# Optimization experiments

Hardware: AMD Instinct MI355X
Metric: run time of the kernel (lower is better)

The kernel has to match this reference:

```python
import jax, jax.numpy as jnp
import numpy as np

EPS = 1e-5
K = 20

def lrelu(x):
    return jnp.where(x >= 0, x, 0.2 * x)

def in2d(x):  # [B,C,N,k] instance norm over (N,k), no affine, biased var
    m = jnp.mean(x, axis=(2, 3), keepdims=True)
    v = jnp.var(x, axis=(2, 3), keepdims=True)
    return (x - m) * jax.lax.rsqrt(v + EPS)

def in1d(x):  # [B,C,N] instance norm over N
    m = jnp.mean(x, axis=2, keepdims=True)
    v = jnp.var(x, axis=2, keepdims=True)
    return (x - m) * jax.lax.rsqrt(v + EPS)

def knn_idx(x, k):  # x: [B,C,N]; uses only first 3 channels (as original)
    p = x[:, :3, :]
    inner = -2.0 * jnp.einsum('bcn,bcm->bnm', p, p)
    xx = jnp.sum(p * p, axis=1)  # [B,N]
    pd = -xx[:, :, None] - inner - xx[:, None, :]  # negative squared dist [B,N,N]
    return jax.lax.top_k(pd, k)[1]  # [B,N,k]

def graph_feature(x, k):  # x: [B,C,N] -> [B,2C,N,k]
    idx = knn_idx(x, k)
    xT = jnp.transpose(x, (0, 2, 1))  # [B,N,C]
    feat = jax.vmap(lambda t, i: t[i])(xT, idx)  # [B,N,k,C]
    center = xT[:, :, None, :]
    out = jnp.concatenate([feat - center, jnp.broadcast_to(center, feat.shape)], axis=3)
    return jnp.transpose(out, (0, 3, 1, 2))  # [B,2C,N,k]

def conv2d1(w, x):  # 1x1 conv2d: w [O,C], x [B,C,N,k]
    return jnp.einsum('oc,bcnk->bonk', w, x)

def conv1d1(w, x):  # 1x1 conv1d: w [O,C], x [B,C,N]
    return jnp.einsum('oc,bcn->bon', w, x)

def setup_inputs() -> dict:
    key = jax.random.key(0)
    ks = jax.random.split(key, 10)
    def w(k, o, c):
        return jax.random.normal(k, (o, c), dtype=jnp.float32) * np.float32(1.0 / np.sqrt(c))
    return {
        'x':  jax.random.normal(ks[0], (4, 4096, 4), dtype=jnp.float32),
        'w1': w(ks[1], 64, 8),
        'w2': w(ks[2], 64, 64),
        'w3': w(ks[3], 64, 128),
        'w4': w(ks[4], 64, 64),
        'w5': w(ks[5], 64, 128),
        'w6': w(ks[6], 1024, 192),
        'w7': w(ks[7], 512, 1216),
        'w8': w(ks[8], 256, 512),
        'w9': w(ks[9], 2, 256),
    }

def reference(x, w1, w2, w3, w4, w5, w6, w7, w8, w9):
    xt = jnp.transpose(x, (0, 2, 1))  # [B,4,N]
    num_points = xt.shape[2]
    # EdgeConv block 1
    f = graph_feature(xt, K)                     # [B,8,N,k]
    h = lrelu(in2d(conv2d1(w1, f)))
    h = lrelu(in2d(conv2d1(w2, h)))
    x1 = jnp.max(h, axis=-1)                     # [B,64,N]
    # EdgeConv block 2
    f = graph_feature(x1, K)                     # [B,128,N,k]
    h = lrelu(in2d(conv2d1(w3, f)))
    h = lrelu(in2d(conv2d1(w4, h)))
    x2 = jnp.max(h, axis=-1)
    # EdgeConv block 3
    f = graph_feature(x2, K)
    h = lrelu(in2d(conv2d1(w5, f)))
    x3 = jnp.max(h, axis=-1)
    # global embedding
    cat = jnp.concatenate([x1, x2, x3], axis=1)  # [B,192,N]
    g = lrelu(in1d(conv1d1(w6, cat)))            # [B,1024,N]
    g = jnp.max(g, axis=-1, keepdims=True)       # [B,1024,1]
    g = jnp.broadcast_to(g, (g.shape[0], g.shape[1], num_points))
    h = jnp.concatenate([g, x1, x2, x3], axis=1) # [B,1216,N]
    h = lrelu(in1d(conv1d1(w7, h)))
    h = lrelu(in1d(conv1d1(w8, h)))
    # dropout identity (eval mode)
    out = conv1d1(w9, h)                         # [B,2,N]
    return jnp.transpose(out, (0, 2, 1))         # [B,N,2]
```

## Files before the change

kernel.cpp:

```cpp
#include <hip/hip_runtime.h>
#include <hip/hip_fp16.h>
#include <math.h>

constexpr int BB  = 4;
constexpr int NN  = 4096;
constexpr int KK  = 20;
constexpr int NKK = NN * KK;
constexpr int TPOS = BB * NKK;
constexpr int NMASK = NN - 1;

#define DEVFN __device__ __forceinline__

DEVFN float lrelu_f(float v) { return v >= 0.f ? v : 0.2f * v; }
DEVFN unsigned fenc(float f) { unsigned u = __float_as_uint(f); return (u & 0x80000000u) ? ~u : (u | 0x80000000u); }
DEVFN float fdec(unsigned k) { unsigned u = (k & 0x80000000u) ? (k & 0x7fffffffu) : ~k; return __uint_as_float(u); }

template<int CSTRIDE>
__global__ __launch_bounds__(256) void knn_kernel(const float* __restrict__ xin, int* __restrict__ idxout)
{
    __shared__ float sx[NN], sy[NN], sz[NN];
    __shared__ unsigned sdist[NN];
    __shared__ unsigned shist[256];
    __shared__ unsigned scollv[256];
    __shared__ unsigned long long scoll64[128];
    __shared__ unsigned sres[2];
    __shared__ unsigned scnt[2];
    const int tid = threadIdx.x;
    const int b  = blockIdx.x >> 8;
    const int q0 = (blockIdx.x & 255) * 16;
    for (int i = tid; i < NN; i += 256) {
        const float4 rc = *reinterpret_cast<const float4*>(xin + (size_t)(b*NN + i) * CSTRIDE);
        sx[i] = rc.x; sy[i] = rc.y; sz[i] = rc.z;
    }

    for (int qq = 0; qq < 16; ++qq) {
        __syncthreads();
        shist[tid] = 0;
        if (tid == 0) { scnt[0] = 0; scnt[1] = 0; }
        const int qi = q0 + qq;
        const float qx = sx[qi], qy = sy[qi], qz = sz[qi];
        const float nxx = -__fadd_rn(__fadd_rn(__fmul_rn(qx,qx), __fmul_rn(qy,qy)), __fmul_rn(qz,qz));
        __syncthreads();
#pragma unroll
        for (int i = 0; i < NN/256; ++i) {
            const int m = tid + (i << 8);
            float cx = sx[m], cy = sy[m], cz = sz[m];
            float cw  = __fadd_rn(__fadd_rn(__fmul_rn(cx,cx), __fmul_rn(cy,cy)), __fmul_rn(cz,cz));
            float dot = __fadd_rn(__fadd_rn(__fmul_rn(qx,cx), __fmul_rn(qy,cy)), __fmul_rn(qz,cz));
            float pd  = __fsub_rn(__fsub_rn(nxx, __fmul_rn(-2.f, dot)), cw);
            unsigned u = fenc(pd);
            sdist[m] = u;
            atomicAdd(&shist[u >> 24], 1u);
        }
        __syncthreads();
        if (tid < 64) {
            const int base = 255 - tid*4;
            unsigned h0 = shist[base], h1 = shist[base-1], h2 = shist[base-2], h3 = shist[base-3];
            unsigned s = h0 + h1 + h2 + h3;
            unsigned c = s;
#pragma unroll
            for (int off = 1; off < 64; off <<= 1) { unsigned t = __shfl_up(c, off, 64); if (tid >= off) c += t; }
            unsigned cprev = c - s;
            if (c >= KK && cprev < KK) {
                unsigned cc = cprev; int bb = base;
                if (cc + h0 < KK) { cc += h0; bb = base-1;
                    if (cc + h1 < KK) { cc += h1; bb = base-2;
                        if (cc + h2 < KK) { cc += h2; bb = base-3; } } }
                sres[0] = (unsigned)bb; sres[1] = KK - cc;
            }
        }
        __syncthreads();
        const unsigned b0 = sres[0], K1 = sres[1];
        shist[tid] = 0;
        __syncthreads();
#pragma unroll
        for (int i = 0; i < NN/256; ++i) {
            unsigned u = sdist[tid + (i << 8)];
            if ((u >> 24) == b0) atomicAdd(&shist[(u >> 16) & 255u], 1u);
        }
        __syncthreads();
        if (tid < 64) {
            const int base = 255 - tid*4;
            unsigned h0 = shist[base], h1 = shist[base-1], h2 = shist[base-2], h3 = shist[base-3];
            unsigned s = h0 + h1 + h2 + h3;
            unsigned c = s;
#pragma unroll
            for (int off = 1; off < 64; off <<= 1) { unsigned t = __shfl_up(c, off, 64); if (tid >= off) c += t; }
            unsigned cprev = c - s;
            if (c >= K1 && cprev < K1) {
                unsigned cc = cprev; int bb = base;
                if (cc + h0 < K1) { cc += h0; bb = base-1;
                    if (cc + h1 < K1) { cc += h1; bb = base-2;
                        if (cc + h2 < K1) { cc += h2; bb = base-3; } } }
                sres[0] = (unsigned)bb; sres[1] = K1 - cc;
            }
        }
        __syncthreads();
        const unsigned prefix16 = (b0 << 8) | sres[0];
        const unsigned K2 = sres[1];
#pragma unroll
        for (int i = 0; i < NN/256; ++i) {
            unsigned u = sdist[tid + (i << 8)];
            if ((u >> 16) == prefix16) {
                unsigned pos = atomicAdd(&scnt[0], 1u);
                if (pos < 256u) scollv[pos] = u;
            }
        }
        __syncthreads();
        {
            int cb = (int)scnt[0]; if (cb > 256) cb = 256;
            if (tid < cb) {
                unsigned v = scollv[tid];
                unsigned ng = 0, ne = 0;
                for (int j = 0; j < cb; ++j) {
                    unsigned w = scollv[j];
                    ng += (w > v); ne += (w == v);
                }
                if (ng < K2 && ng + ne >= K2) sres[0] = v;
            }
        }
        __syncthreads();
        const unsigned W = sres[0];
#pragma unroll
        for (int i = 0; i < NN/256; ++i) {
            const int m = tid + (i << 8);
            unsigned u = sdist[m];
            if (u >= W) {
                unsigned pos = atomicAdd(&scnt[1], 1u);
                if (pos < 128u) scoll64[pos] = ((unsigned long long)u << 32) | (unsigned)(NN-1 - m);
            }
        }
        __syncthreads();
        {
            int c2 = (int)scnt[1]; if (c2 > 128) c2 = 128;
            if (tid < c2) {
                unsigned long long kv = scoll64[tid];
                int rank = 0;
                for (int j = 0; j < c2; ++j) rank += (scoll64[j] > kv);
                if (rank < KK) {
                    int* op = idxout + ((size_t)(b*NN + qi)) * KK;
                    op[rank] = (NN-1) - (int)(kv & 0xFFFFFFFFull);
                }
            }
        }
    }
}

template<int CINH, int CSTRIDE>
__global__ __launch_bounds__(64) void uv_kernel(const float* __restrict__ xin, const float* __restrict__ w,
                                                float* __restrict__ ub, float* __restrict__ vb)
{
    __shared__ float sp[32][CINH];
    const int lane = threadIdx.x;
    float wa[CINH], wd[CINH];
#pragma unroll
    for (int c = 0; c < CINH; ++c) {
        float a = w[lane*(2*CINH) + c];
        wa[c] = a;
        wd[c] = w[lane*(2*CINH) + CINH + c] - a;
    }
    const int p0 = blockIdx.x * 32;
    for (int i = lane; i < 32*CINH; i += 64) {
        int pi = i / CINH, c = i % CINH;
        sp[pi][c] = xin[(size_t)(p0 + pi)*CSTRIDE + c];
    }
    __syncthreads();
    for (int pi = 0; pi < 32; ++pi) {
        float au = 0.f, av = 0.f;
#pragma unroll
        for (int c = 0; c < CINH; ++c) {
            float xv = sp[pi][c];
            au = fmaf(wa[c], xv, au);
            av = fmaf(wd[c], xv, av);
        }
        ub[(size_t)(p0 + pi)*64 + lane] = au;
        vb[(size_t)(p0 + pi)*64 + lane] = av;
    }
}

template<bool STOREMAX>
__global__ __launch_bounds__(64) void gstat_kernel(const float* __restrict__ ub, const float* __restrict__ vb,
    const int* __restrict__ idx, float* __restrict__ xraw,
    double* __restrict__ ssum, double* __restrict__ ssq)
{
    const int lane = threadIdx.x;
    const int g0 = blockIdx.x * 8;
    const int b = g0 / NN;
    double lsum = 0.0, lsq = 0.0;
    for (int ni = 0; ni < 8; ++ni) {
        const int g = g0 + ni;
        const float v = vb[(size_t)g*64 + lane];
        float vmax = -INFINITY;
        for (int k = 0; k < KK; ++k) {
            const int j = idx[(size_t)g*KK + k] & NMASK;
            float o = ub[(size_t)(b*NN + j)*64 + lane] + v;
            if constexpr (STOREMAX) vmax = fmaxf(vmax, o);
            lsum += (double)o; lsq += (double)o*(double)o;
        }
        if constexpr (STOREMAX) xraw[(size_t)g*64 + lane] = vmax;
    }
    atomicAdd(&ssum[b*64+lane], lsum);
    atomicAdd(&ssq [b*64+lane], lsq);
}

__global__ __launch_bounds__(64) void s1b_kernel(const float* __restrict__ x, const int* __restrict__ idx,
    const float* __restrict__ w1, const float* __restrict__ w2,
    const float* __restrict__ m1, const float* __restrict__ r1,
    float* __restrict__ xraw, double* __restrict__ ssum, double* __restrict__ ssq)
{
    __shared__ float sh[64];
    const int lane = threadIdx.x;
    float wr1[8];
#pragma unroll
    for (int c = 0; c < 8; ++c) wr1[c] = w1[lane*8 + c];
    float wr2[64];
#pragma unroll
    for (int c = 0; c < 64; ++c) wr2[c] = w2[lane*64 + c];
    const int g0 = blockIdx.x * 8;
    const int b = g0 / NN;
    const float mm = m1[b*64+lane], rr = r1[b*64+lane];
    double lsum = 0.0, lsq = 0.0;
    for (int ni = 0; ni < 8; ++ni) {
        const int g = g0 + ni;
        const float4 ct = *reinterpret_cast<const float4*>(x + (size_t)g*4);
        float vmax = -INFINITY;
        for (int k = 0; k < KK; ++k) {
            const int j = idx[(size_t)g*KK + k] & NMASK;
            const float4 nb = *reinterpret_cast<const float4*>(x + (size_t)(b*NN + j)*4);
            float o1 = wr1[0]*(nb.x-ct.x) + wr1[1]*(nb.y-ct.y) + wr1[2]*(nb.z-ct.z) + wr1[3]*(nb.w-ct.w)
                     + wr1[4]*ct.x + wr1[5]*ct.y + wr1[6]*ct.z + wr1[7]*ct.w;
            float h = lrelu_f((o1 - mm) * rr);
            __syncthreads();
            sh[lane] = h;
            __syncthreads();
            float acc = 0.f;
#pragma unroll
            for (int c = 0; c < 64; c += 4) {
                const float4 hv = *reinterpret_cast<const float4*>(&sh[c]);
                acc += wr2[c]*hv.x + wr2[c+1]*hv.y + wr2[c+2]*hv.z + wr2[c+3]*hv.w;
            }
            vmax = fmaxf(vmax, acc);
            lsum += (double)acc; lsq += (double)acc*(double)acc;
        }
        xraw[(size_t)g*64 + lane] = vmax;
    }
    atomicAdd(&ssum[b*64+lane], lsum);
    atomicAdd(&ssq [b*64+lane], lsq);
}

__global__ __launch_bounds__(64) void s2b_kernel(const float* __restrict__ xin, const int* __restrict__ idx,
    const float* __restrict__ w3, const float* __restrict__ w4,
    const float* __restrict__ m3, const float* __restrict__ r3,
    float* __restrict__ xraw, double* __restrict__ ssum, double* __restrict__ ssq)
{
    __shared__ float sf[128];
    __shared__ float sh[64];
    const int lane = threadIdx.x;
    float wr3[128];
#pragma unroll
    for (int c = 0; c < 128; ++c) wr3[c] = w3[lane*128 + c];
    float wr4[64];
#pragma unroll
    for (int c = 0; c < 64; ++c) wr4[c] = w4[lane*64 + c];
    const int g0 = blockIdx.x * 8;
    const int b = g0 / NN;
    const float mm = m3[b*64+lane], rr = r3[b*64+lane];
    double lsum = 0.0, lsq = 0.0;
    for (int ni = 0; ni < 8; ++ni) {
        const int g = g0 + ni;
        const float ctl = xin[(size_t)g*64 + lane];
        float vmax = -INFINITY;
        for (int k = 0; k < KK; ++k) {
            const int j = idx[(size_t)g*KK + k] & NMASK;
            const float nbl = xin[(size_t)(b*NN + j)*64 + lane];
            __syncthreads();
            sf[lane] = nbl - ctl;
            sf[64+lane] = ctl;
            __syncthreads();
            float o3 = 0.f;
#pragma unroll
            for (int c = 0; c < 128; c += 4) {
                const float4 fv = *reinterpret_cast<const float4*>(&sf[c]);
                o3 += wr3[c]*fv.x + wr3[c+1]*fv.y + wr3[c+2]*fv.z + wr3[c+3]*fv.w;
            }
            float h = lrelu_f((o3 - mm) * rr);
            __syncthreads();
            sh[lane] = h;
            __syncthreads();
            float acc = 0.f;
#pragma unroll
            for (int c = 0; c < 64; c += 4) {
                const float4 hv = *reinterpret_cast<const float4*>(&sh[c]);
                acc += wr4[c]*hv.x + wr4[c+1]*hv.y + wr4[c+2]*hv.z + wr4[c+3]*hv.w;
            }
            vmax = fmaxf(vmax, acc);
            lsum += (double)acc; lsq += (double)acc*(double)acc;
        }
        xraw[(size_t)g*64 + lane] = vmax;
    }
    atomicAdd(&ssum[b*64+lane], lsum);
    atomicAdd(&ssq [b*64+lane], lsq);
}

__global__ void fin_kernel(const double* __restrict__ ssum, const double* __restrict__ ssq,
                           float* __restrict__ meanp, float* __restrict__ rstdp, int total, double invn)
{
    int t = blockIdx.x*256 + threadIdx.x;
    if (t >= total) return;
    double m = ssum[t]*invn;
    double v = ssq[t]*invn - m*m;
    meanp[t] = (float)m;
    rstdp[t] = (float)(1.0 / sqrt(v + 1e-5));
}

__global__ void finx_kernel(float* __restrict__ xv, const float* __restrict__ m, const float* __restrict__ r)
{
    int t = blockIdx.x*256 + threadIdx.x;
    int c0 = (t & 15) * 4;
    int b = t >> 16;
    float4 v = *reinterpret_cast<float4*>(xv + (size_t)t*4);
    v.x = lrelu_f((v.x - m[b*64+c0+0]) * r[b*64+c0+0]);
    v.y = lrelu_f((v.y - m[b*64+c0+1]) * r[b*64+c0+1]);
    v.z = lrelu_f((v.z - m[b*64+c0+2]) * r[b*64+c0+2]);
    v.w = lrelu_f((v.w - m[b*64+c0+3]) * r[b*64+c0+3]);
    *reinterpret_cast<float4*>(xv + (size_t)t*4) = v;
}

__global__ void transw_kernel(const float* __restrict__ w, float* __restrict__ wT, int O, int C, int rs, int off)
{
    int t = blockIdx.x*256 + threadIdx.x;
    if (t >= O*C) return;
    int o = t % O, c = t / O;
    wT[t] = w[(size_t)o*rs + off + c];
}

__global__ __launch_bounds__(256) void conv6_kernel(
    const float* __restrict__ x1, const float* __restrict__ x2, const float* __restrict__ x3,
    const float* __restrict__ wT, double* __restrict__ s6sum, double* __restrict__ s6sq, unsigned* __restrict__ s6max)
{
    __shared__ float si[32][192];
    const int b = blockIdx.z, nbase = blockIdx.x*32;
    const int o = blockIdx.y*256 + threadIdx.x;
    for (int i = threadIdx.x; i < 32*192; i += 256) {
        int nl = i/192, c = i%192;
        size_t base = (size_t)(b*NN + nbase + nl)*64;
        si[nl][c] = (c < 64) ? x1[base + c] : (c < 128) ? x2[base + c - 64] : x3[base + c - 128];
    }
    __syncthreads();
    float acc[32];
#pragma unroll
    for (int n = 0; n < 32; ++n) acc[n] = 0.f;
    for (int c = 0; c < 192; ++c) {
        float wv = wT[(size_t)c*1024 + o];
#pragma unroll
        for (int n = 0; n < 32; ++n) acc[n] = fmaf(wv, si[n][c], acc[n]);
    }
    double ps = 0.0, pq = 0.0; float pm = -INFINITY;
#pragma unroll
    for (int n = 0; n < 32; ++n) { ps += (double)acc[n]; pq += (double)acc[n]*(double)acc[n]; pm = fmaxf(pm, acc[n]); }
    atomicAdd(&s6sum[b*1024+o], ps);
    atomicAdd(&s6sq [b*1024+o], pq);
    atomicMax(&s6max[b*1024+o], fenc(pm));
}

__global__ void gfin_kernel(const double* __restrict__ s6sum, const double* __restrict__ s6sq,
                            const unsigned* __restrict__ s6max, float* __restrict__ g)
{
    int t = blockIdx.x*256 + threadIdx.x;
    double m = s6sum[t] * (1.0/4096.0);
    double v = s6sq[t] * (1.0/4096.0) - m*m;
    float rs = (float)(1.0 / sqrt(v + 1e-5));
    g[t] = lrelu_f((fdec(s6max[t]) - (float)m) * rs);
}

__global__ __launch_bounds__(256) void gbias_kernel(const float* __restrict__ w7, const float* __restrict__ g,
                                                    float* __restrict__ gbias)
{
    const int b = blockIdx.y;
    const int o = blockIdx.x*256 + threadIdx.x;
    const float* wr = w7 + (size_t)o*1216;
    const float* gv = g + b*1024;
    float acc = 0.f;
    for (int c = 0; c < 1024; c += 4) {
        float4 wv = *reinterpret_cast<const float4*>(&wr[c]);
        float4 gg = *reinterpret_cast<const float4*>(&gv[c]);
        acc = fmaf(wv.x, gg.x, fmaf(wv.y, gg.y, fmaf(wv.z, gg.z, fmaf(wv.w, gg.w, acc))));
    }
    gbias[b*512+o] = acc;
}

__global__ __launch_bounds__(256) void conv7a_kernel(
    const float* __restrict__ x1, const float* __restrict__ x2, const float* __restrict__ x3,
    const float* __restrict__ wT, const float* __restrict__ gbias,
    __half* __restrict__ out7h, double* __restrict__ ssum, double* __restrict__ ssq)
{
    __shared__ float si[32][192];
    const int b = blockIdx.z, nbase = blockIdx.x*32;
    const int o = blockIdx.y*256 + threadIdx.x;
    for (int i = threadIdx.x; i < 32*192; i += 256) {
        int nl = i/192, c = i%192;
        size_t base = (size_t)(b*NN + nbase + nl)*64;
        si[nl][c] = (c < 64) ? x1[base + c] : (c < 128) ? x2[base + c - 64] : x3[base + c - 128];
    }
    __syncthreads();
    float acc[32];
    const float gb = gbias[b*512 + o];
#pragma unroll
    for (int n = 0; n < 32; ++n) acc[n] = gb;
    for (int c = 0; c < 192; ++c) {
        float wv = wT[(size_t)c*512 + o];
#pragma unroll
        for (int n = 0; n < 32; ++n) acc[n] = fmaf(wv, si[n][c], acc[n]);
    }
    double ps = 0.0, pq = 0.0;
#pragma unroll
    for (int n = 0; n < 32; ++n) {
        out7h[(size_t)(b*NN + nbase + n)*512 + o] = __float2half(acc[n]);
        ps += (double)acc[n]; pq += (double)acc[n]*(double)acc[n];
    }
    atomicAdd(&ssum[b*512+o], ps);
    atomicAdd(&ssq [b*512+o], pq);
}

__global__ __launch_bounds__(256) void conv8k_kernel(
    const __half* __restrict__ out7h, const float* __restrict__ m7, const float* __restrict__ r7,
    const float* __restrict__ wT8,
    float* __restrict__ out8, double* __restrict__ ssum, double* __restrict__ ssq)
{
    __shared__ float h7[16][512];
    const int b = blockIdx.y, nbase = blockIdx.x*16;
    const int tid = threadIdx.x;
    for (int i = tid; i < 16*512; i += 256) {
        int nl = i >> 9, c = i & 511;
        float v = __half2float(out7h[(size_t)(b*NN + nbase + nl)*512 + c]);
        h7[nl][c] = lrelu_f((v - m7[b*512+c]) * r7[b*512+c]);
    }
    __syncthreads();
    const int o = tid;
    float acc8[16];
#pragma unroll
    for (int n = 0; n < 16; ++n) acc8[n] = 0.f;
    for (int c = 0; c < 512; ++c) {
        float wv = wT8[(size_t)c*256 + o];
#pragma unroll
        for (int n = 0; n < 16; ++n) acc8[n] = fmaf(wv, h7[n][c], acc8[n]);
    }
    double ps = 0.0, pq = 0.0;
#pragma unroll
    for (int n = 0; n < 16; ++n) {
        out8[(size_t)(b*NN + nbase + n)*256 + o] = acc8[n];
        ps += (double)acc8[n]; pq += (double)acc8[n]*(double)acc8[n];
    }
    atomicAdd(&ssum[b*256+o], ps);
    atomicAdd(&ssq [b*256+o], pq);
}

__global__ __launch_bounds__(256) void conv9_kernel(const float* __restrict__ in8,
    const float* __restrict__ meanp, const float* __restrict__ rstdp,
    const float* __restrict__ w9, float* __restrict__ outp)
{
    const int lane = threadIdx.x & 63, wv = threadIdx.x >> 6;
    const int ng = blockIdx.x*4 + wv;
    const int b = ng / NN;
    const int c0 = lane*4;
    const float4 v4 = *reinterpret_cast<const float4*>(&in8[(size_t)ng*256 + c0]);
    float vv[4] = {v4.x, v4.y, v4.z, v4.w};
    float a0 = 0.f, a1 = 0.f;
#pragma unroll
    for (int i = 0; i < 4; ++i) {
        int c = c0 + i;
        float a = lrelu_f((vv[i] - meanp[b*256+c]) * rstdp[b*256+c]);
        a0 = fmaf(w9[c],     a, a0);
        a1 = fmaf(w9[256+c], a, a1);
    }
#pragma unroll
    for (int off = 32; off > 0; off >>= 1) {
        a0 += __shfl_down(a0, off, 64);
        a1 += __shfl_down(a1, off, 64);
    }
    if (lane == 0) { outp[(size_t)ng*2 + 0] = a0; outp[(size_t)ng*2 + 1] = a1; }
}

extern "C" void kernel_launch(void* const* d_in, const int* in_sizes, int n_in,
                              void* d_out, int out_size, void* d_ws, size_t ws_size,
                              hipStream_t stream)
{
    const float* x  = (const float*)d_in[0];
    const float* w1 = (const float*)d_in[1];
    const float* w2 = (const float*)d_in[2];
    const float* w3 = (const float*)d_in[3];
    const float* w4 = (const float*)d_in[4];
    const float* w5 = (const float*)d_in[5];
    const float* w6 = (const float*)d_in[6];
    const float* w7 = (const float*)d_in[7];
    const float* w8 = (const float*)d_in[8];
    const float* w9 = (const float*)d_in[9];
    float* outp = (float*)d_out;

    char* ws = (char*)d_ws;
    size_t off = 0;
    auto alloc = [&](size_t bytes) -> void* {
        void* p = ws + off;
        off = (off + bytes + 255) & ~(size_t)255;
        return p;
    };
    double* dstats = (double*)alloc((size_t)16896 * 8);
    unsigned* u6max = (unsigned*)alloc((size_t)4096 * 4);
    float* fstats = (float*)alloc((size_t)14848 * 4);
    int*   idxb  = (int*)  alloc((size_t)TPOS * 4);
    float* wT6   = (float*)alloc((size_t)1024*192*4);
    float* wT7   = (float*)alloc((size_t)512*192*4);
    float* wT8   = (float*)alloc((size_t)256*512*4);
    char*  sc17  = (char*) alloc((size_t)BB*NN*512*2);
    float* ubuf  = (float*)sc17;
    float* vbuf  = (float*)(sc17 + (size_t)BB*NN*64*4);
    __half* out7h = (__half*)sc17;
    float* x1v   = (float*)alloc((size_t)BB*NN*64*4);
    float* x2v   = (float*)alloc((size_t)BB*NN*64*4);
    float* x3v   = (float*)alloc((size_t)BB*NN*64*4);
    float* out8  = (float*)alloc((size_t)BB*NN*256*4);

    double* d1 = dstats;           double* d2 = dstats + 512;
    double* d3 = dstats + 1024;    double* d4 = dstats + 1536;
    double* d5 = dstats + 2048;
    double* d6sum = dstats + 2560; double* d6sq = d6sum + 4096;
    double* d7sum = dstats + 10752; double* d7sq = d7sum + 2048;
    double* d8sum = dstats + 14848; double* d8sq = d8sum + 1024;
    float* m1 = fstats;        float* r1 = fstats + 256;
    float* m2 = fstats + 512;  float* r2 = fstats + 768;
    float* m3 = fstats + 1024; float* r3 = fstats + 1280;
    float* m4 = fstats + 1536; float* r4 = fstats + 1792;
    float* m5 = fstats + 2048; float* r5 = fstats + 2304;
    float* g  = fstats + 2560;
    float* m7 = fstats + 6656; float* r7 = fstats + 8704;
    float* gbias = fstats + 10752;
    float* m8 = fstats + 12800; float* r8 = fstats + 13824;

    hipMemsetAsync(dstats, 0, (size_t)16896*8 + (size_t)4096*4, stream);

    transw_kernel<<<768, 256, 0, stream>>>(w6, wT6, 1024, 192, 192, 0);
    transw_kernel<<<384, 256, 0, stream>>>(w7, wT7, 512, 192, 1216, 1024);
    transw_kernel<<<512, 256, 0, stream>>>(w8, wT8, 256, 512, 512, 0);

    knn_kernel<4><<<1024, 256, 0, stream>>>(x, idxb);
    uv_kernel<4, 4><<<512, 64, 0, stream>>>(x, w1, ubuf, vbuf);
    gstat_kernel<false><<<2048, 64, 0, stream>>>(ubuf, vbuf, idxb, nullptr, d1, d1+256);
    fin_kernel<<<1, 256, 0, stream>>>(d1, d1+256, m1, r1, 256, 1.0/81920.0);
    s1b_kernel<<<2048, 64, 0, stream>>>(x, idxb, w1, w2, m1, r1, x1v, d2, d2+256);
    fin_kernel<<<1, 256, 0, stream>>>(d2, d2+256, m2, r2, 256, 1.0/81920.0);
    finx_kernel<<<1024, 256, 0, stream>>>(x1v, m2, r2);

    knn_kernel<64><<<1024, 256, 0, stream>>>(x1v, idxb);
    uv_kernel<64, 64><<<512, 64, 0, stream>>>(x1v, w3, ubuf, vbuf);
    gstat_kernel<false><<<2048, 64, 0, stream>>>(ubuf, vbuf, idxb, nullptr, d3, d3+256);
    fin_kernel<<<1, 256, 0, stream>>>(d3, d3+256, m3, r3, 256, 1.0/81920.0);
    s2b_kernel<<<2048, 64, 0, stream>>>(x1v, idxb, w3, w4, m3, r3, x2v, d4, d4+256);
    fin_kernel<<<1, 256, 0, stream>>>(d4, d4+256, m4, r4, 256, 1.0/81920.0);
    finx_kernel<<<1024, 256, 0, stream>>>(x2v, m4, r4);

    knn_kernel<64><<<1024, 256, 0, stream>>>(x2v, idxb);
    uv_kernel<64, 64><<<512, 64, 0, stream>>>(x2v, w5, ubuf, vbuf);
    gstat_kernel<true><<<2048, 64, 0, stream>>>(ubuf, vbuf, idxb, x3v, d5, d5+256);
    fin_kernel<<<1, 256, 0, stream>>>(d5, d5+256, m5, r5, 256, 1.0/81920.0);
    finx_kernel<<<1024, 256, 0, stream>>>(x3v, m5, r5);

    conv6_kernel<<<dim3(128, 4, 4), 256, 0, stream>>>(x1v, x2v, x3v, wT6, d6sum, d6sq, u6max);
    gfin_kernel<<<16, 256, 0, stream>>>(d6sum, d6sq, u6max, g);
    gbias_kernel<<<dim3(2, 4), 256, 0, stream>>>(w7, g, gbias);

    conv7a_kernel<<<dim3(128, 2, 4), 256, 0, stream>>>(x1v, x2v, x3v, wT7, gbias, out7h, d7sum, d7sq);
    fin_kernel<<<8, 256, 0, stream>>>(d7sum, d7sq, m7, r7, 2048, 1.0/4096.0);
    conv8k_kernel<<<dim3(256, 4), 256, 0, stream>>>(out7h, m7, r7, wT8, out8, d8sum, d8sq);
    fin_kernel<<<4, 256, 0, stream>>>(d8sum, d8sq, m8, r8, 1024, 1.0/4096.0);
    conv9_kernel<<<4096, 256, 0, stream>>>(out8, m8, r8, w9, outp);
}
```

Measured before the change: 1.855 ms.

## Drop global embedding branch cancelled by instance norm; keep kNN keys in registers

```diff
diff --git a/kernel.cpp b/kernel.cpp
--- a/kernel.cpp
+++ b/kernel.cpp
@@ -13,13 +13,11 @@
 
 DEVFN float lrelu_f(float v) { return v >= 0.f ? v : 0.2f * v; }
 DEVFN unsigned fenc(float f) { unsigned u = __float_as_uint(f); return (u & 0x80000000u) ? ~u : (u | 0x80000000u); }
-DEVFN float fdec(unsigned k) { unsigned u = (k & 0x80000000u) ? (k & 0x7fffffffu) : ~k; return __uint_as_float(u); }
 
 template<int CSTRIDE>
 __global__ __launch_bounds__(256) void knn_kernel(const float* __restrict__ xin, int* __restrict__ idxout)
 {
     __shared__ float sx[NN], sy[NN], sz[NN];
-    __shared__ unsigned sdist[NN];
     __shared__ unsigned shist[256];
     __shared__ unsigned scollv[256];
     __shared__ unsigned long long scoll64[128];
@@ -41,6 +39,7 @@
         const float qx = sx[qi], qy = sy[qi], qz = sz[qi];
         const float nxx = -__fadd_rn(__fadd_rn(__fmul_rn(qx,qx), __fmul_rn(qy,qy)), __fmul_rn(qz,qz));
         __syncthreads();
+        unsigned ukey[NN/256];
 #pragma unroll
         for (int i = 0; i < NN/256; ++i) {
             const int m = tid + (i << 8);
@@ -49,7 +48,7 @@
             float dot = __fadd_rn(__fadd_rn(__fmul_rn(qx,cx), __fmul_rn(qy,cy)), __fmul_rn(qz,cz));
             float pd  = __fsub_rn(__fsub_rn(nxx, __fmul_rn(-2.f, dot)), cw);
             unsigned u = fenc(pd);
-            sdist[m] = u;
+            ukey[i] = u;
             atomicAdd(&shist[u >> 24], 1u);
         }
         __syncthreads();
@@ -75,7 +74,7 @@
         __syncthreads();
 #pragma unroll
         for (int i = 0; i < NN/256; ++i) {
-            unsigned u = sdist[tid + (i << 8)];
+            unsigned u = ukey[i];
             if ((u >> 24) == b0) atomicAdd(&shist[(u >> 16) & 255u], 1u);
         }
         __syncthreads();
@@ -100,7 +99,7 @@
         const unsigned K2 = sres[1];
 #pragma unroll
         for (int i = 0; i < NN/256; ++i) {
-            unsigned u = sdist[tid + (i << 8)];
+            unsigned u = ukey[i];
             if ((u >> 16) == prefix16) {
                 unsigned pos = atomicAdd(&scnt[0], 1u);
                 if (pos < 256u) scollv[pos] = u;
@@ -124,7 +123,7 @@
 #pragma unroll
         for (int i = 0; i < NN/256; ++i) {
             const int m = tid + (i << 8);
-            unsigned u = sdist[m];
+            unsigned u = ukey[i];
             if (u >= W) {
                 unsigned pos = atomicAdd(&scnt[1], 1u);
                 if (pos < 128u) scoll64[pos] = ((unsigned long long)u << 32) | (unsigned)(NN-1 - m);
@@ -334,9 +333,10 @@
     wT[t] = w[(size_t)o*rs + off + c];
 }
 
-__global__ __launch_bounds__(256) void conv6_kernel(
+__global__ __launch_bounds__(256) void conv7a_kernel(
     const float* __restrict__ x1, const float* __restrict__ x2, const float* __restrict__ x3,
-    const float* __restrict__ wT, double* __restrict__ s6sum, double* __restrict__ s6sq, unsigned* __restrict__ s6max)
+    const float* __restrict__ wT,
+    __half* __restrict__ out7h, double* __restrict__ ssum, double* __restrict__ ssq)
 {
     __shared__ float si[32][192];
     const int b = blockIdx.z, nbase = blockIdx.x*32;
@@ -351,63 +351,6 @@
 #pragma unroll
     for (int n = 0; n < 32; ++n) acc[n] = 0.f;
     for (int c = 0; c < 192; ++c) {
-        float wv = wT[(size_t)c*1024 + o];
-#pragma unroll
-        for (int n = 0; n < 32; ++n) acc[n] = fmaf(wv, si[n][c], acc[n]);
-    }
-    double ps = 0.0, pq = 0.0; float pm = -INFINITY;
-#pragma unroll
-    for (int n = 0; n < 32; ++n) { ps += (double)acc[n]; pq += (double)acc[n]*(double)acc[n]; pm = fmaxf(pm, acc[n]); }
-    atomicAdd(&s6sum[b*1024+o], ps);
-    atomicAdd(&s6sq [b*1024+o], pq);
-    atomicMax(&s6max[b*1024+o], fenc(pm));
-}
-
-__global__ void gfin_kernel(const double* __restrict__ s6sum, const double* __restrict__ s6sq,
-                            const unsigned* __restrict__ s6max, float* __restrict__ g)
-{
-    int t = blockIdx.x*256 + threadIdx.x;
-    double m = s6sum[t] * (1.0/4096.0);
-    double v = s6sq[t] * (1.0/4096.0) - m*m;
-    float rs = (float)(1.0 / sqrt(v + 1e-5));
-    g[t] = lrelu_f((fdec(s6max[t]) - (float)m) * rs);
-}
-
-__global__ __launch_bounds__(256) void gbias_kernel(const float* __restrict__ w7, const float* __restrict__ g,
-                                                    float* __restrict__ gbias)
-{
-    const int b = blockIdx.y;
-    const int o = blockIdx.x*256 + threadIdx.x;
-    const float* wr = w7 + (size_t)o*1216;
-    const float* gv = g + b*1024;
-    float acc = 0.f;
-    for (int c = 0; c < 1024; c += 4) {
-        float4 wv = *reinterpret_cast<const float4*>(&wr[c]);
-        float4 gg = *reinterpret_cast<const float4*>(&gv[c]);
-        acc = fmaf(wv.x, gg.x, fmaf(wv.y, gg.y, fmaf(wv.z, gg.z, fmaf(wv.w, gg.w, acc))));
-    }
-    gbias[b*512+o] = acc;
-}
-
-__global__ __launch_bounds__(256) void conv7a_kernel(
-    const float* __restrict__ x1, const float* __restrict__ x2, const float* __restrict__ x3,
-    const float* __restrict__ wT, const float* __restrict__ gbias,
-    __half* __restrict__ out7h, double* __restrict__ ssum, double* __restrict__ ssq)
-{
-    __shared__ float si[32][192];
-    const int b = blockIdx.z, nbase = blockIdx.x*32;
-    const int o = blockIdx.y*256 + threadIdx.x;
-    for (int i = threadIdx.x; i < 32*192; i += 256) {
-        int nl = i/192, c = i%192;
-        size_t base = (size_t)(b*NN + nbase + nl)*64;
-        si[nl][c] = (c < 64) ? x1[base + c] : (c < 128) ? x2[base + c - 64] : x3[base + c - 128];
-    }
-    __syncthreads();
-    float acc[32];
-    const float gb = gbias[b*512 + o];
-#pragma unroll
-    for (int n = 0; n < 32; ++n) acc[n] = gb;
-    for (int c = 0; c < 192; ++c) {
         float wv = wT[(size_t)c*512 + o];
 #pragma unroll
         for (int n = 0; n < 32; ++n) acc[n] = fmaf(wv, si[n][c], acc[n]);
@@ -491,7 +434,6 @@
     const float* w3 = (const float*)d_in[3];
     const float* w4 = (const float*)d_in[4];
     const float* w5 = (const float*)d_in[5];
-    const float* w6 = (const float*)d_in[6];
     const float* w7 = (const float*)d_in[7];
     const float* w8 = (const float*)d_in[8];
     const float* w9 = (const float*)d_in[9];
@@ -508,7 +450,6 @@
     unsigned* u6max = (unsigned*)alloc((size_t)4096 * 4);
     float* fstats = (float*)alloc((size_t)14848 * 4);
     int*   idxb  = (int*)  alloc((size_t)TPOS * 4);
-    float* wT6   = (float*)alloc((size_t)1024*192*4);
     float* wT7   = (float*)alloc((size_t)512*192*4);
     float* wT8   = (float*)alloc((size_t)256*512*4);
     char*  sc17  = (char*) alloc((size_t)BB*NN*512*2);
@@ -520,10 +461,10 @@
     float* x3v   = (float*)alloc((size_t)BB*NN*64*4);
     float* out8  = (float*)alloc((size_t)BB*NN*256*4);
 
+    (void)u6max;
     double* d1 = dstats;           double* d2 = dstats + 512;
     double* d3 = dstats + 1024;    double* d4 = dstats + 1536;
     double* d5 = dstats + 2048;
-    double* d6sum = dstats + 2560; double* d6sq = d6sum + 4096;
     double* d7sum = dstats + 10752; double* d7sq = d7sum + 2048;
     double* d8sum = dstats + 14848; double* d8sq = d8sum + 1024;
     float* m1 = fstats;        float* r1 = fstats + 256;
@@ -531,14 +472,11 @@
     float* m3 = fstats + 1024; float* r3 = fstats + 1280;
     float* m4 = fstats + 1536; float* r4 = fstats + 1792;
     float* m5 = fstats + 2048; float* r5 = fstats + 2304;
-    float* g  = fstats + 2560;
     float* m7 = fstats + 6656; float* r7 = fstats + 8704;
-    float* gbias = fstats + 10752;
     float* m8 = fstats + 12800; float* r8 = fstats + 13824;
 
     hipMemsetAsync(dstats, 0, (size_t)16896*8 + (size_t)4096*4, stream);
 
-    transw_kernel<<<768, 256, 0, stream>>>(w6, wT6, 1024, 192, 192, 0);
     transw_kernel<<<384, 256, 0, stream>>>(w7, wT7, 512, 192, 1216, 1024);
     transw_kernel<<<512, 256, 0, stream>>>(w8, wT8, 256, 512, 512, 0);
 
@@ -564,11 +502,7 @@
     fin_kernel<<<1, 256, 0, stream>>>(d5, d5+256, m5, r5, 256, 1.0/81920.0);
     finx_kernel<<<1024, 256, 0, stream>>>(x3v, m5, r5);
 
-    conv6_kernel<<<dim3(128, 4, 4), 256, 0, stream>>>(x1v, x2v, x3v, wT6, d6sum, d6sq, u6max);
-    gfin_kernel<<<16, 256, 0, stream>>>(d6sum, d6sq, u6max, g);
-    gbias_kernel<<<dim3(2, 4), 256, 0, stream>>>(w7, g, gbias);
-
-    conv7a_kernel<<<dim3(128, 2, 4), 256, 0, stream>>>(x1v, x2v, x3v, wT7, gbias, out7h, d7sum, d7sq);
+    conv7a_kernel<<<dim3(128, 2, 4), 256, 0, stream>>>(x1v, x2v, x3v, wT7, out7h, d7sum, d7sq);
     fin_kernel<<<8, 256, 0, stream>>>(d7sum, d7sq, m7, r7, 2048, 1.0/4096.0);
     conv8k_kernel<<<dim3(256, 4), 256, 0, stream>>>(out7h, m7, r7, wT8, out8, d8sum, d8sq);
     fin_kernel<<<4, 256, 0, stream>>>(d8sum, d8sq, m8, r8, 1024, 1.0/4096.0);
```

Result: faster. 1.559 ms (median of 2 runs) (-16.0%).
